# Kernel tuning notes

Measured on AMD Instinct MI355X. Metric: run time of the kernel, lower is better.

## Reference

```python
import jax, jax.numpy as jnp
import numpy as np

N_TAU = 100  # number of steps per delay interval: dt = tau / N_TAU = 0.01 * tau


def _F(x, y, t, params):
    # Delay-logistic vector field: x'(t) = theta0 * x(t) * (1 - theta1 * x(t - tau))
    return params[0] * x * (1.0 - params[1] * y)


def setup_inputs() -> dict:
    key = jax.random.key(0)
    k1, = jax.random.split(key, 1)
    d = 32768
    x_0 = jax.random.uniform(k1, (d,), dtype=jnp.float32)  # positive ICs, stable dynamics
    tau = jnp.ones((1,), dtype=jnp.float32)
    params = jnp.ones((2,), dtype=jnp.float32)  # theta0, theta1
    N = 1000  # T = N * dt = 10 * tau
    return {"x_0": x_0, "tau": tau, "params": params, "N": N}


def reference(x_0, tau, params, N):
    # Forward-Euler DDE solve with constant history x(t) = x_0 for t in [-tau, 0].
    d = x_0.shape[0]
    dt = 0.01 * tau[0]
    dtype = x_0.dtype
    traj0 = jnp.zeros((N + 1, d), dtype=dtype).at[0].set(x_0)  # rows are time steps

    def step(traj, i):
        x_i = traj[i]                                            # current state [d]
        # delayed state x(t_i - tau): history (= x_0) for the first N_TAU steps
        y_i = jnp.where(i >= N_TAU, traj[jnp.maximum(i - N_TAU, 0)], x_0)
        t_i = i.astype(dtype) * dt
        x_next = x_i + dt * _F(x_i, y_i, t_i, params)
        return traj.at[i + 1].set(x_next), None

    traj, _ = jax.lax.scan(step, traj0, jnp.arange(N))
    # match torch convention: kth COLUMN is the state at the kth time step -> [d, N+1]
    return traj.T
```

## Files before the change

kernel.cpp:

```cpp
#include <hip/hip_runtime.h>


constexpr int NT   = 1000;
constexpr int NTAU = 100;
constexpr int NGRP = NT / NTAU;
constexpr int NP1  = NT + 1;
constexpr int COMP = 64;
constexpr int LSTR = NTAU + 1;
constexpr int NCW  = 3;

#define R5(F,B)   F(B) F((B)+1) F((B)+2) F((B)+3) F((B)+4)
#define R25(F,B)  R5(F,B) R5(F,(B)+5) R5(F,(B)+10) R5(F,(B)+15) R5(F,(B)+20)
#define R50(F,B)  R25(F,B) R25(F,(B)+25)
#define R100(F)   R50(F,0) R50(F,50)

#define LDS_ORDER() do {                                    \
    __builtin_amdgcn_sched_barrier(0);                      \
    asm volatile("s_waitcnt lgkmcnt(0)" ::: "memory");      \
    __builtin_amdgcn_sched_barrier(0);                      \
} while (0)

__global__ __launch_bounds__(256, 1)
void ndde_kernel(const float* __restrict__ x0,
                 const float* __restrict__ tau,
                 const float* __restrict__ params,
                 float* __restrict__ out)
{
    __shared__ float buf[2][COMP][LSTR];
    __shared__ int   prodf;
    __shared__ int   consf[NCW];
    const int tid  = threadIdx.x;
    const int wid  = tid >> 6;
    const int lane = tid & 63;
    const int jbase = (int)blockIdx.x * COMP;

    const float dt = 0.01f * tau[0];
    const float a  = dt * params[0];
    const float q  = -(a * params[1]);
    const float p  = 1.0f + a;

    if (tid == 0) { prodf = 0; consf[0] = 0; consf[1] = 0; consf[2] = 0; }
    __syncthreads();

    volatile int* vprod = &prodf;
    volatile int* vcons = consf;

    if (wid == 0) {
        float x = x0[jbase + lane];
        float h[NTAU];
#define INIT_H(K) h[(K)] = x;
        R100(INIT_H)
#define STEP(K) { const float y_ = h[(K)]; h[(K)] = x; x *= fmaf(q, y_, p); }
#define STG(K)  bp[(K)] = h[(K)];

#pragma clang loop unroll(disable)
        for (int g = 0; g < NGRP; ++g) {
            if (g >= 2) {
                while (vcons[0] < g - 1 || vcons[1] < g - 1 || vcons[2] < g - 1)
                    __builtin_amdgcn_s_sleep(1);
                LDS_ORDER();
            }
            R100(STEP)
            float* bp = &buf[g & 1][lane][0];
            R100(STG)
            LDS_ORDER();
            *vprod = g + 1;
        }
        out[(jbase + lane) * NP1 + NT] = x;
    } else {
        const int cw = wid - 1;
        float* gpb = out + jbase * NP1 + lane;
#pragma clang loop unroll(disable)
        for (int g = 0; g < NGRP; ++g) {
            while (*vprod < g + 1)
                __builtin_amdgcn_s_sleep(1);
            LDS_ORDER();
            const float* bb = &buf[g & 1][0][0];
            float* gp = gpb + g * NTAU;
            for (int r = cw; r < COMP; r += NCW) {
                const float* lr = bb + r * LSTR;
                float* rp = gp + r * NP1;
                rp[0] = lr[lane];
                if (lane < NTAU - 64)
                    rp[64] = lr[64 + lane];
            }
            LDS_ORDER();
            vcons[cw] = g + 1;
        }
    }
}

extern "C" void kernel_launch(void* const* d_in, const int* in_sizes, int n_in,
                              void* d_out, int out_size, void* d_ws, size_t ws_size,
                              hipStream_t stream) {
    const float* x0     = (const float*)d_in[0];
    const float* tau    = (const float*)d_in[1];
    const float* params = (const float*)d_in[2];
    float* out = (float*)d_out;
    const int d = in_sizes[0];
    const int nblocks = d / COMP;
    ndde_kernel<<<nblocks, 256, 0, stream>>>(x0, tau, params, out);
}
```

Baseline: 33.21 us.

## Double phase size to 200 steps and give copier waves contiguous row ranges

The producer wave now runs 200 Euler steps per phase, staging two 100-step chunks into a wider LDS buffer. This halves the number of producer/consumer handshakes and spin-waits. The three copier waves each take a contiguous block of rows instead of interleaving. They issue all LDS loads for two rows before the global stores to raise memory-level parallelism. LDS use doubles, and the staging stores between the two step blocks may lengthen the producer's critical path.

```diff
diff --git a/kernel.cpp b/kernel.cpp
--- a/kernel.cpp
+++ b/kernel.cpp
@@ -3,10 +3,11 @@
 
 constexpr int NT   = 1000;
 constexpr int NTAU = 100;
-constexpr int NGRP = NT / NTAU;
+constexpr int NPH  = 5;
+constexpr int PCOL = 200;
 constexpr int NP1  = NT + 1;
 constexpr int COMP = 64;
-constexpr int LSTR = NTAU + 1;
+constexpr int LSTR = PCOL + 1;
 constexpr int NCW  = 3;
 
 #define R5(F,B)   F(B) F((B)+1) F((B)+2) F((B)+3) F((B)+4)
@@ -51,41 +52,59 @@
 #define INIT_H(K) h[(K)] = x;
         R100(INIT_H)
 #define STEP(K) { const float y_ = h[(K)]; h[(K)] = x; x *= fmaf(q, y_, p); }
-#define STG(K)  bp[(K)] = h[(K)];
+#define STG0(K) bp[(K)] = h[(K)];
+#define STG1(K) bp[100+(K)] = h[(K)];
 
 #pragma clang loop unroll(disable)
-        for (int g = 0; g < NGRP; ++g) {
-            if (g >= 2) {
-                while (vcons[0] < g - 1 || vcons[1] < g - 1 || vcons[2] < g - 1)
+        for (int ph = 0; ph < NPH; ++ph) {
+            if (ph >= 2) {
+                while (vcons[0] < ph - 1 || vcons[1] < ph - 1 || vcons[2] < ph - 1)
                     __builtin_amdgcn_s_sleep(1);
                 LDS_ORDER();
             }
+            float* bp = &buf[ph & 1][lane][0];
             R100(STEP)
-            float* bp = &buf[g & 1][lane][0];
-            R100(STG)
+            R100(STG0)
+            R100(STEP)
+            R100(STG1)
             LDS_ORDER();
-            *vprod = g + 1;
+            *vprod = ph + 1;
         }
         out[(jbase + lane) * NP1 + NT] = x;
     } else {
-        const int cw = wid - 1;
-        float* gpb = out + jbase * NP1 + lane;
+        const int cw    = wid - 1;
+        const int start = (cw == 0) ? 0 : (cw == 1) ? 22 : 43;
+        const int cnt   = (cw == 0) ? 22 : 21;
+        const int lane8 = (lane < 8) ? lane : 7;
+        float* gpb = out + (jbase + start) * NP1 + lane;
+
 #pragma clang loop unroll(disable)
-        for (int g = 0; g < NGRP; ++g) {
-            while (*vprod < g + 1)
+        for (int ph = 0; ph < NPH; ++ph) {
+            while (*vprod < ph + 1)
                 __builtin_amdgcn_s_sleep(1);
             LDS_ORDER();
-            const float* bb = &buf[g & 1][0][0];
-            float* gp = gpb + g * NTAU;
-            for (int r = cw; r < COMP; r += NCW) {
-                const float* lr = bb + r * LSTR;
-                float* rp = gp + r * NP1;
-                rp[0] = lr[lane];
-                if (lane < NTAU - 64)
-                    rp[64] = lr[64 + lane];
+            const float* bb = &buf[ph & 1][start][0];
+            float* gp = gpb + ph * PCOL;
+
+            for (int r = 0; r < cnt; r += 2) {
+                const int r1 = (r + 1 < cnt) ? r + 1 : r;
+                const float* la = bb + r  * LSTR;
+                const float* lb = bb + r1 * LSTR;
+                float a0 = la[lane], a1 = la[64 + lane], a2 = la[128 + lane];
+                float a3 = la[192 + lane8];
+                float b0 = lb[lane], b1 = lb[64 + lane], b2 = lb[128 + lane];
+                float b3 = lb[192 + lane8];
+                float* ra = gp + r  * NP1;
+                float* rb = gp + r1 * NP1;
+                ra[0] = a0; ra[64] = a1; ra[128] = a2;
+                if (lane < 8) ra[192] = a3;
+                if (r1 != r) {
+                    rb[0] = b0; rb[64] = b1; rb[128] = b2;
+                    if (lane < 8) rb[192] = b3;
+                }
             }
             LDS_ORDER();
-            vcons[cw] = g + 1;
+            vcons[cw] = ph + 1;
         }
     }
 }
```

Result: faster. 31.51 us (-5.1%).
